# Kernel tuning notes

Hardware: AMD Instinct MI355X
Metric: run time of the kernel (lower is better)

The kernel has to match this reference:

```python
import jax, jax.numpy as jnp
import numpy as np

D_STATE = 16
DT_RANK = 48
D_CONV = 4
EPS = 1e-5


def rmsnorm(x, w):
    return x * jax.lax.rsqrt(jnp.mean(x * x, axis=-1, keepdims=True) + EPS) * w


def causal_dw_conv(u, w, b):
    # u: [B,T,D], w: [D,K] depthwise causal kernel, b: [D]
    B, T, D = u.shape
    K = w.shape[1]
    up = jnp.pad(u, ((0, 0), (K - 1, 0), (0, 0)))
    acc = jnp.zeros_like(u)
    for k in range(K):  # K=4, tiny fixed loop
        acc = acc + up[:, k:k + T, :] * w[:, k]
    return acc + b


def mamba_mixer(h, ipw, cw, cb, xpw, dpw, dpb, alog, dpar, opw):
    # h: [B,T,d_model]
    B, T, _ = h.shape
    xz = h @ ipw.T                       # [B,T,2*d_inner]
    u, z = jnp.split(xz, 2, axis=-1)     # each [B,T,d_inner]
    u = jax.nn.silu(causal_dw_conv(u, cw, cb))
    xp = u @ xpw.T                       # [B,T,dt_rank+2*d_state]
    dt = xp[..., :DT_RANK]
    Bm = xp[..., DT_RANK:DT_RANK + D_STATE]
    Cm = xp[..., DT_RANK + D_STATE:]
    delta = jax.nn.softplus(dt @ dpw.T + dpb)      # [B,T,d_inner]
    A = -jnp.exp(alog)                              # [d_inner, d_state], negative
    dA = jnp.exp(delta[..., None] * A)              # [B,T,d_inner,d_state] in (0,1)
    dBu = (delta * u)[..., None] * Bm[:, :, None, :]
    # time-major for scan
    dA_t = jnp.moveaxis(dA, 1, 0)
    dBu_t = jnp.moveaxis(dBu, 1, 0)
    C_t = jnp.moveaxis(Cm, 1, 0)

    def step(hst, inp):
        a, bu, c = inp
        hst = a * hst + bu                          # [B,d_inner,d_state]
        y = jnp.einsum('bdn,bn->bd', hst, c)
        return hst, y

    h0 = jnp.zeros((B, u.shape[-1], D_STATE), u.dtype)
    _, ys = jax.lax.scan(step, h0, (dA_t, dBu_t, C_t))
    y = jnp.moveaxis(ys, 0, 1) + u * dpar           # skip via D
    y = y * jax.nn.silu(z)                          # gate
    return y @ opw.T                                # [B,T,d_model]


def setup_inputs() -> dict:
    key = jax.random.key(0)
    ks = jax.random.split(key, 16)
    L, d_model, d_inner = 4, 768, 1536
    B, C, T = 4, 256, 512
    s = 0.02
    return {
        'x': jax.random.normal(ks[0], (B, C, T), jnp.float32),
        'in_proj_w': jax.random.normal(ks[1], (L, 2 * d_inner, d_model), jnp.float32) * s,
        'conv_w': jax.random.normal(ks[2], (L, d_inner, D_CONV), jnp.float32) * 0.3,
        'conv_b': jnp.zeros((L, d_inner), jnp.float32),
        'x_proj_w': jax.random.normal(ks[3], (L, DT_RANK + 2 * D_STATE, d_inner), jnp.float32) * s,
        'dt_proj_w': jax.random.normal(ks[4], (L, d_inner, DT_RANK), jnp.float32) * 0.1,
        'dt_proj_b': jax.random.normal(ks[5], (L, d_inner), jnp.float32) * 0.1 - 4.0,
        'A_log': jax.random.uniform(ks[6], (L, d_inner, D_STATE), jnp.float32, 0.0, 1.5),
        'D_param': jax.random.uniform(ks[7], (L, d_inner), jnp.float32),
        'out_proj_w': jax.random.normal(ks[8], (L, d_model, d_inner), jnp.float32) * s,
        'norm_w': jnp.ones((L, d_model), jnp.float32),
        'norm_f_w': jnp.ones((d_model,), jnp.float32),
        'inp_w': jax.random.normal(ks[9], (d_model, C), jnp.float32) * s,
        'inp_b': jnp.zeros((d_model,), jnp.float32),
        'cls_w': jax.random.normal(ks[10], (10, d_model), jnp.float32) * s,
        'cls_b': jnp.zeros((10,), jnp.float32),
    }


def reference(x, in_proj_w, conv_w, conv_b, x_proj_w, dt_proj_w, dt_proj_b,
              A_log, D_param, out_proj_w, norm_w, norm_f_w,
              inp_w, inp_b, cls_w, cls_b):
    # x: (B, C, T) -> (B, T, C)
    xt = jnp.transpose(x, (0, 2, 1))
    h = xt @ inp_w.T + inp_b                # [B,T,d_model]
    hidden = h
    residual = None
    L = in_proj_w.shape[0]
    for l in range(L):
        residual = hidden if residual is None else hidden + residual
        normed = rmsnorm(residual, norm_w[l])
        hidden = mamba_mixer(normed, in_proj_w[l], conv_w[l], conv_b[l],
                             x_proj_w[l], dt_proj_w[l], dt_proj_b[l],
                             A_log[l], D_param[l], out_proj_w[l])
    residual = hidden + residual
    hidden = rmsnorm(residual, norm_f_w)
    pooled = hidden.mean(axis=1)            # [B,d_model]
    logits = pooled @ cls_w.T + cls_b       # [B,num_labels]
    return logits
```

## Files before the change

kernel.cpp:

```cpp
#include <hip/hip_runtime.h>
#include <math.h>

#define D_MODEL 768
#define D_INNER 1536
#define B_SZ 4
#define T_SZ 512
#define ROWS (B_SZ*T_SZ)
#define XP_N 80
#define CH 16
#define CT 32
#define XS 8
#define XKC (D_INNER/XS)
#define OS 4
#define OKC (D_INNER/OS)
#define MN_OUT (ROWS*768)

typedef __attribute__((ext_vector_type(8))) short bf16x8;
typedef __attribute__((ext_vector_type(4))) float f32x4;

__device__ __forceinline__ float sigmoidf_(float x){ return 1.0f/(1.0f+__expf(-x)); }
__device__ __forceinline__ float siluf_(float x){ return x*sigmoidf_(x); }
__device__ __forceinline__ unsigned short f2bf(float f){
  unsigned u = __builtin_bit_cast(unsigned, f);
  u = (u + 0x7FFFu + ((u >> 16) & 1u)) >> 16;
  return (unsigned short)u;
}

__global__ void transpose_x(const float* __restrict__ x, float* __restrict__ xt){
  __shared__ float s[32][33];
  int b = blockIdx.z;
  int t0 = blockIdx.x*32, c0 = blockIdx.y*32;
  int tx = threadIdx.x, ty = threadIdx.y;
  s[ty][tx] = x[((size_t)b*256 + (c0+ty))*512 + (t0+tx)];
  __syncthreads();
  xt[((size_t)b*512 + (t0+ty))*256 + (c0+tx)] = s[tx][ty];
}

__global__ __launch_bounds__(256) void cast2_bf16(
    const float* __restrict__ in1, unsigned short* __restrict__ o1, int n1, int nb1,
    const float* __restrict__ in2, unsigned short* __restrict__ o2, int n2)
{
  const float* in; unsigned short* o; int i4;
  if ((int)blockIdx.x < nb1){ in = in1; o = o1; i4 = (blockIdx.x*256 + threadIdx.x)*4; if (i4 >= n1) return; }
  else { in = in2; o = o2; i4 = ((blockIdx.x-nb1)*256 + threadIdx.x)*4; if (i4 >= n2) return; }
  float4 v = *(const float4*)(in + i4);
  ushort4 r;
  r.x = f2bf(v.x); r.y = f2bf(v.y); r.z = f2bf(v.z); r.w = f2bf(v.w);
  *(ushort4*)(o + i4) = r;
}

#define LDP 40
__global__ __launch_bounds__(256) void gemm_bf16(
    const unsigned short* __restrict__ A, const unsigned short* __restrict__ Wb,
    float* __restrict__ C, int M, int N, int K)
{
  __shared__ unsigned short As[128*LDP];
  __shared__ unsigned short Ws[128*LDP];
  const int tid = threadIdx.x;
  const int bm = blockIdx.y*128, bn = blockIdx.x*128;
  const int wave = tid >> 6, lane = tid & 63;
  const int wm = (wave >> 1)*64, wn = (wave & 1)*64;
  const int fr = lane & 15, quad = lane >> 4;
  f32x4 acc[4][4] = {};
  const int srow = tid >> 1, scol = (tid & 1)*16;
  const unsigned short* Ag = A  + (size_t)(bm + srow)*K + scol;
  const unsigned short* Wg = Wb + (size_t)(bn + srow)*K + scol;
  unsigned short* Asw = As + srow*LDP + scol;
  unsigned short* Wsw = Ws + srow*LDP + scol;

  for (int k0 = 0; k0 < K; k0 += 32){
    float4 av0 = *(const float4*)(Ag + k0);
    float4 av1 = *(const float4*)(Ag + k0 + 8);
    float4 wv0 = *(const float4*)(Wg + k0);
    float4 wv1 = *(const float4*)(Wg + k0 + 8);
    __syncthreads();
    *(float4*)(Asw)     = av0; *(float4*)(Asw + 8) = av1;
    *(float4*)(Wsw)     = wv0; *(float4*)(Wsw + 8) = wv1;
    __syncthreads();
    bf16x8 a[4], b[4];
    #pragma unroll
    for (int i=0;i<4;i++)
      a[i] = *(const bf16x8*)(As + (wm + i*16 + fr)*LDP + quad*8);
    #pragma unroll
    for (int j=0;j<4;j++)
      b[j] = *(const bf16x8*)(Ws + (wn + j*16 + fr)*LDP + quad*8);
    #pragma unroll
    for (int i=0;i<4;i++)
      #pragma unroll
      for (int j=0;j<4;j++)
        acc[i][j] = __builtin_amdgcn_mfma_f32_16x16x32_bf16(a[i], b[j], acc[i][j], 0, 0, 0);
  }
  #pragma unroll
  for (int i=0;i<4;i++){
    #pragma unroll
    for (int r=0;r<4;r++){
      const int row = bm + wm + i*16 + quad*4 + r;
      float* Cp = C + (size_t)row*N + bn + wn + fr;
      #pragma unroll
      for (int j=0;j<4;j++)
        Cp[j*16] = acc[i][j][r];
    }
  }
}

__global__ __launch_bounds__(256) void gemm_bf16_sk(
    const unsigned short* __restrict__ A, const unsigned short* __restrict__ Wb,
    float* __restrict__ P0, float* __restrict__ P1, int M, int N, int K)
{
  __shared__ unsigned short As[128*LDP];
  __shared__ unsigned short Ws[128*LDP];
  const int tid = threadIdx.x;
  const int bm = blockIdx.y*128, bn = blockIdx.x*128;
  const int s = blockIdx.z;
  const int koff = s*OKC;
  const int wave = tid >> 6, lane = tid & 63;
  const int wm = (wave >> 1)*64, wn = (wave & 1)*64;
  const int fr = lane & 15, quad = lane >> 4;
  f32x4 acc[4][4] = {};
  const int srow = tid >> 1, scol = (tid & 1)*16;
  const unsigned short* Ag = A  + (size_t)(bm + srow)*K + koff + scol;
  const unsigned short* Wg = Wb + (size_t)(bn + srow)*K + koff + scol;
  unsigned short* Asw = As + srow*LDP + scol;
  unsigned short* Wsw = Ws + srow*LDP + scol;

  for (int k0 = 0; k0 < OKC; k0 += 32){
    float4 av0 = *(const float4*)(Ag + k0);
    float4 av1 = *(const float4*)(Ag + k0 + 8);
    float4 wv0 = *(const float4*)(Wg + k0);
    float4 wv1 = *(const float4*)(Wg + k0 + 8);
    __syncthreads();
    *(float4*)(Asw)     = av0; *(float4*)(Asw + 8) = av1;
    *(float4*)(Wsw)     = wv0; *(float4*)(Wsw + 8) = wv1;
    __syncthreads();
    bf16x8 a[4], b[4];
    #pragma unroll
    for (int i=0;i<4;i++)
      a[i] = *(const bf16x8*)(As + (wm + i*16 + fr)*LDP + quad*8);
    #pragma unroll
    for (int j=0;j<4;j++)
      b[j] = *(const bf16x8*)(Ws + (wn + j*16 + fr)*LDP + quad*8);
    #pragma unroll
    for (int i=0;i<4;i++)
      #pragma unroll
      for (int j=0;j<4;j++)
        acc[i][j] = __builtin_amdgcn_mfma_f32_16x16x32_bf16(a[i], b[j], acc[i][j], 0, 0, 0);
  }
  float* Cb = (s < 2 ? P0 : P1) + (size_t)(s & 1)*MN_OUT;
  #pragma unroll
  for (int i=0;i<4;i++){
    #pragma unroll
    for (int r=0;r<4;r++){
      const int row = bm + wm + i*16 + quad*4 + r;
      float* Cp = Cb + (size_t)row*N + bn + wn + fr;
      #pragma unroll
      for (int j=0;j<4;j++)
        Cp[j*16] = acc[i][j][r];
    }
  }
}

__global__ __launch_bounds__(256) void reduce_out(
    const float* __restrict__ P0, const float* __restrict__ P1,
    float* __restrict__ C)
{
  const int i = blockIdx.x*256 + threadIdx.x;
  C[i] = (P0[i] + P0[MN_OUT + i]) + (P1[i] + P1[MN_OUT + i]);
}

__global__ __launch_bounds__(256) void sgemm_tn(
    const float* __restrict__ A, int lda,
    const float* __restrict__ W,
    const float* __restrict__ bias,
    float* __restrict__ C, int M, int N, int K, int act)
{
  __shared__ float As[16][64];
  __shared__ float Wsh[16][64];
  const int bm = blockIdx.y*64, bn = blockIdx.x*64;
  const int tid = threadIdx.x;
  const int tx = tid & 15, ty = tid >> 4;
  const int lm = tid & 63, lk = (tid >> 6) << 2;
  float acc[4][4] = {};
  const float* Ap = A + (size_t)(bm+lm)*lda + lk;
  const float* Wp = W + (size_t)(bn+lm)*K + lk;
  const bool wok = (bn+lm) < N;
  for (int k0 = 0; k0 < K; k0 += 16){
    float4 av = *(const float4*)(Ap + k0);
    float4 wv = wok ? *(const float4*)(Wp + k0) : make_float4(0.f,0.f,0.f,0.f);
    As[lk+0][lm]=av.x; As[lk+1][lm]=av.y; As[lk+2][lm]=av.z; As[lk+3][lm]=av.w;
    Wsh[lk+0][lm]=wv.x; Wsh[lk+1][lm]=wv.y; Wsh[lk+2][lm]=wv.z; Wsh[lk+3][lm]=wv.w;
    __syncthreads();
    #pragma unroll
    for (int k = 0; k < 16; k++){
      float a[4], w[4];
      #pragma unroll
      for (int i=0;i<4;i++) a[i] = As[k][ty*4+i];
      #pragma unroll
      for (int j=0;j<4;j++) w[j] = Wsh[k][tx*4+j];
      #pragma unroll
      for (int i=0;i<4;i++)
        #pragma unroll
        for (int j=0;j<4;j++)
          acc[i][j] += a[i]*w[j];
    }
    __syncthreads();
  }
  #pragma unroll
  for (int i=0;i<4;i++){
    const int r = bm + ty*4 + i;
    #pragma unroll
    for (int j=0;j<4;j++){
      const int n = bn + tx*4 + j;
      if (n < N){
        float v = acc[i][j] + (bias ? bias[n] : 0.f);
        if (act == 1){ v = (v > 20.f) ? v : log1pf(__expf(v)); }
        C[(size_t)r*N + n] = v;
      }
    }
  }
}

__global__ __launch_bounds__(256) void sgemm_splitk_xp(
    const float* __restrict__ A, const float* __restrict__ W,
    float* __restrict__ part)
{
  __shared__ float As[16][64];
  __shared__ float Wsh[16][64];
  const int bm = blockIdx.y*64, bn = blockIdx.x*64;
  const int s = blockIdx.z;
  const int koff = s*XKC;
  const int tid = threadIdx.x;
  const int tx = tid & 15, ty = tid >> 4;
  const int lm = tid & 63, lk = (tid >> 6) << 2;
  float acc[4][4] = {};
  const float* Ap = A + (size_t)(bm+lm)*D_INNER + koff + lk;
  const float* Wp = W + (size_t)(bn+lm)*D_INNER + koff + lk;
  const bool wok = (bn+lm) < XP_N;
  for (int k0 = 0; k0 < XKC; k0 += 16){
    float4 av = *(const float4*)(Ap + k0);
    float4 wv = wok ? *(const float4*)(Wp + k0) : make_float4(0.f,0.f,0.f,0.f);
    As[lk+0][lm]=av.x; As[lk+1][lm]=av.y; As[lk+2][lm]=av.z; As[lk+3][lm]=av.w;
    Wsh[lk+0][lm]=wv.x; Wsh[lk+1][lm]=wv.y; Wsh[lk+2][lm]=wv.z; Wsh[lk+3][lm]=wv.w;
    __syncthreads();
    #pragma unroll
    for (int k = 0; k < 16; k++){
      float a[4], w[4];
      #pragma unroll
      for (int i=0;i<4;i++) a[i] = As[k][ty*4+i];
      #pragma unroll
      for (int j=0;j<4;j++) w[j] = Wsh[k][tx*4+j];
      #pragma unroll
      for (int i=0;i<4;i++)
        #pragma unroll
        for (int j=0;j<4;j++)
          acc[i][j] += a[i]*w[j];
    }
    __syncthreads();
  }
  #pragma unroll
  for (int i=0;i<4;i++){
    const int r = bm + ty*4 + i;
    #pragma unroll
    for (int j=0;j<4;j++){
      const int n = bn + tx*4 + j;
      if (n < XP_N)
        part[((size_t)s*ROWS + r)*XP_N + n] = acc[i][j];
    }
  }
}

__global__ __launch_bounds__(256) void reduce_xp(const float* __restrict__ part,
                                                 float* __restrict__ xp){
  const int i = blockIdx.x*256 + threadIdx.x;
  if (i >= ROWS*XP_N) return;
  float s = 0.f;
  #pragma unroll
  for (int c=0;c<XS;c++) s += part[(size_t)c*ROWS*XP_N + i];
  xp[i] = s;
}

__global__ __launch_bounds__(256) void add_rmsnorm(
    float* __restrict__ resid, const float* __restrict__ add,
    const float* __restrict__ w, float* __restrict__ out,
    unsigned short* __restrict__ obf)
{
  const int row = blockIdx.x;
  const int tid = threadIdx.x;
  float v[3];
  float ss = 0.f;
  #pragma unroll
  for (int i=0;i<3;i++){
    const int c = tid + i*256;
    float r = resid[(size_t)row*768 + c];
    if (add) r += add[(size_t)row*768 + c];
    v[i] = r;
    ss += r*r;
  }
  #pragma unroll
  for (int off=32; off>=1; off>>=1) ss += __shfl_xor(ss, off);
  __shared__ float sred[4];
  const int lane = tid & 63, wv = tid >> 6;
  if (lane == 0) sred[wv] = ss;
  __syncthreads();
  const float tot = sred[0]+sred[1]+sred[2]+sred[3];
  const float scale = rsqrtf(tot*(1.0f/768.0f) + 1e-5f);
  #pragma unroll
  for (int i=0;i<3;i++){
    const int c = tid + i*256;
    if (add) resid[(size_t)row*768 + c] = v[i];
    const float o = v[i]*scale*w[c];
    if (obf) obf[(size_t)row*768 + c] = f2bf(o);
    else     out[(size_t)row*768 + c] = o;
  }
}

__global__ __launch_bounds__(256) void conv_silu(
    const float* __restrict__ xz, const float* __restrict__ cw,
    const float* __restrict__ cb, float* __restrict__ uo)
{
  const int idx = blockIdx.x*256 + threadIdx.x;
  if (idx >= ROWS*D_INNER) return;
  const int d = idx % D_INNER;
  const int row = idx / D_INNER;
  const int t = row & (T_SZ-1);
  float acc = cb[d];
  #pragma unroll
  for (int k=0;k<4;k++){
    const int tt = t - 3 + k;
    if (tt >= 0)
      acc += xz[(size_t)(row - 3 + k)*3072 + d] * cw[d*4 + k];
  }
  uo[idx] = siluf_(acc);
}

__global__ __launch_bounds__(256) void scan_pass1(
    const float* __restrict__ delta, const float* __restrict__ u,
    const float* __restrict__ xp, const float* __restrict__ alog,
    float* __restrict__ Pend, float* __restrict__ Hend)
{
  const int d = blockIdx.x*256 + threadIdx.x;
  const int b = blockIdx.y, c = blockIdx.z;
  float4 t0 = *(const float4*)(alog + d*16 + 0);
  float4 t1 = *(const float4*)(alog + d*16 + 4);
  float4 t2 = *(const float4*)(alog + d*16 + 8);
  float4 t3 = *(const float4*)(alog + d*16 + 12);
  float Av[16] = {t0.x,t0.y,t0.z,t0.w,t1.x,t1.y,t1.z,t1.w,
                  t2.x,t2.y,t2.z,t2.w,t3.x,t3.y,t3.z,t3.w};
  float h[16], P[16];
  #pragma unroll
  for (int n=0;n<16;n++){ Av[n] = -__expf(Av[n]); h[n]=0.f; P[n]=1.f; }
  const size_t row0 = (size_t)b*T_SZ + (size_t)c*CT;
  const float* dp = delta + row0*D_INNER + d;
  const float* up = u     + row0*D_INNER + d;
  const float* bp = xp    + row0*XP_N + 48;
  for (int t=0;t<CT;t++){
    const float dv = dp[(size_t)t*D_INNER];
    const float uv = up[(size_t)t*D_INNER];
    const float4 B0 = *(const float4*)(bp + (size_t)t*XP_N);
    const float4 B1 = *(const float4*)(bp + (size_t)t*XP_N + 4);
    const float4 B2 = *(const float4*)(bp + (size_t)t*XP_N + 8);
    const float4 B3 = *(const float4*)(bp + (size_t)t*XP_N + 12);
    const float Bv[16] = {B0.x,B0.y,B0.z,B0.w,B1.x,B1.y,B1.z,B1.w,
                          B2.x,B2.y,B2.z,B2.w,B3.x,B3.y,B3.z,B3.w};
    const float du = dv*uv;
    #pragma unroll
    for (int n=0;n<16;n++){
      const float dA = __expf(dv*Av[n]);
      P[n] *= dA;
      h[n] = dA*h[n] + du*Bv[n];
    }
  }
  float* Pp = Pend + ((size_t)(b*CH+c)*D_INNER + d)*16;
  float* Hp = Hend + ((size_t)(b*CH+c)*D_INNER + d)*16;
  *(float4*)(Pp+ 0) = make_float4(P[0],P[1],P[2],P[3]);
  *(float4*)(Pp+ 4) = make_float4(P[4],P[5],P[6],P[7]);
  *(float4*)(Pp+ 8) = make_float4(P[8],P[9],P[10],P[11]);
  *(float4*)(Pp+12) = make_float4(P[12],P[13],P[14],P[15]);
  *(float4*)(Hp+ 0) = make_float4(h[0],h[1],h[2],h[3]);
  *(float4*)(Hp+ 4) = make_float4(h[4],h[5],h[6],h[7]);
  *(float4*)(Hp+ 8) = make_float4(h[8],h[9],h[10],h[11]);
  *(float4*)(Hp+12) = make_float4(h[12],h[13],h[14],h[15]);
}

__global__ __launch_bounds__(256) void scan_combine(
    const float* __restrict__ Pend, const float* __restrict__ Hend,
    float* __restrict__ Hin)
{
  const int gid = blockIdx.x*256 + threadIdx.x;
  const int b = gid / (D_INNER*16);
  const int r = gid % (D_INNER*16);
  const size_t base = (size_t)b*CH*D_INNER*16 + r;
  const size_t step = (size_t)D_INNER*16;
  float h = 0.f;
  Hin[base] = 0.f;
  for (int c=0; c<CH-1; c++){
    h = Pend[base + (size_t)c*step]*h + Hend[base + (size_t)c*step];
    Hin[base + (size_t)(c+1)*step] = h;
  }
}

__global__ __launch_bounds__(256) void scan_pass3(
    const float* __restrict__ delta, const float* __restrict__ u,
    const float* __restrict__ xp, const float* __restrict__ xz,
    const float* __restrict__ alog, const float* __restrict__ Dp,
    const float* __restrict__ Hin, unsigned short* __restrict__ yb)
{
  const int d = blockIdx.x*256 + threadIdx.x;
  const int b = blockIdx.y, c = blockIdx.z;
  float4 t0 = *(const float4*)(alog + d*16 + 0);
  float4 t1 = *(const float4*)(alog + d*16 + 4);
  float4 t2 = *(const float4*)(alog + d*16 + 8);
  float4 t3 = *(const float4*)(alog + d*16 + 12);
  float Av[16] = {t0.x,t0.y,t0.z,t0.w,t1.x,t1.y,t1.z,t1.w,
                  t2.x,t2.y,t2.z,t2.w,t3.x,t3.y,t3.z,t3.w};
  #pragma unroll
  for (int n=0;n<16;n++) Av[n] = -__expf(Av[n]);
  const float* Hp = Hin + ((size_t)(b*CH+c)*D_INNER + d)*16;
  float4 h0 = *(const float4*)(Hp+0);
  float4 h1 = *(const float4*)(Hp+4);
  float4 h2 = *(const float4*)(Hp+8);
  float4 h3 = *(const float4*)(Hp+12);
  float h[16] = {h0.x,h0.y,h0.z,h0.w,h1.x,h1.y,h1.z,h1.w,
                 h2.x,h2.y,h2.z,h2.w,h3.x,h3.y,h3.z,h3.w};
  const float Dv = Dp[d];
  const size_t row0 = (size_t)b*T_SZ + (size_t)c*CT;
  const float* dp = delta + row0*D_INNER + d;
  const float* up = u     + row0*D_INNER + d;
  const float* bp = xp    + row0*XP_N + 48;
  const float* cp = xp    + row0*XP_N + 64;
  const float* zp = xz    + row0*3072 + 1536 + d;
  unsigned short* yp = yb + row0*D_INNER + d;
  for (int t=0;t<CT;t++){
    const float dv = dp[(size_t)t*D_INNER];
    const float uv = up[(size_t)t*D_INNER];
    const float zv = zp[(size_t)t*3072];
    const float4 B0 = *(const float4*)(bp + (size_t)t*XP_N);
    const float4 B1 = *(const float4*)(bp + (size_t)t*XP_N + 4);
    const float4 B2 = *(const float4*)(bp + (size_t)t*XP_N + 8);
    const float4 B3 = *(const float4*)(bp + (size_t)t*XP_N + 12);
    const float4 C0 = *(const float4*)(cp + (size_t)t*XP_N);
    const float4 C1 = *(const float4*)(cp + (size_t)t*XP_N + 4);
    const float4 C2 = *(const float4*)(cp + (size_t)t*XP_N + 8);
    const float4 C3 = *(const float4*)(cp + (size_t)t*XP_N + 12);
    const float Bv[16] = {B0.x,B0.y,B0.z,B0.w,B1.x,B1.y,B1.z,B1.w,
                          B2.x,B2.y,B2.z,B2.w,B3.x,B3.y,B3.z,B3.w};
    const float Cv[16] = {C0.x,C0.y,C0.z,C0.w,C1.x,C1.y,C1.z,C1.w,
                          C2.x,C2.y,C2.z,C2.w,C3.x,C3.y,C3.z,C3.w};
    const float du = dv*uv;
    float p = 0.f;
    #pragma unroll
    for (int n=0;n<16;n++){
      const float dA = __expf(dv*Av[n]);
      h[n] = dA*h[n] + du*Bv[n];
      p += h[n]*Cv[n];
    }
    yp[(size_t)t*D_INNER] = f2bf((p + uv*Dv)*siluf_(zv));
  }
}

__global__ __launch_bounds__(256) void pool_partial(const float* __restrict__ normed,
                                                    float* __restrict__ part){
  const int i = blockIdx.x*256 + threadIdx.x;
  const int s = blockIdx.y;
  const int b = i / 768, m = i % 768;
  float sum = 0.f;
  const float* p = normed + ((size_t)b*T_SZ + s*32)*768 + m;
  #pragma unroll
  for (int t=0; t<32; t++) sum += p[(size_t)t*768];
  part[s*3072 + i] = sum;
}

__global__ void pool_final(const float* __restrict__ part, float* __restrict__ pooled){
  const int i = blockIdx.x*256 + threadIdx.x;
  if (i >= 3072) return;
  float s = 0.f;
  #pragma unroll
  for (int c=0;c<16;c++) s += part[c*3072 + i];
  pooled[i] = s * (1.0f/T_SZ);
}

__global__ void cls_head(const float* __restrict__ pooled, const float* __restrict__ cw,
                         const float* __restrict__ cb, float* __restrict__ out){
  const int o = blockIdx.x % 10, b = blockIdx.x / 10;
  const int lane = threadIdx.x;
  float s = 0.f;
  for (int k = lane; k < 768; k += 64) s += pooled[b*768 + k]*cw[o*768 + k];
  #pragma unroll
  for (int off=32; off>=1; off>>=1) s += __shfl_xor(s, off);
  if (lane == 0) out[b*10 + o] = s + cb[o];
}

extern "C" void kernel_launch(void* const* d_in, const int* in_sizes, int n_in,
                              void* d_out, int out_size, void* d_ws, size_t ws_size,
                              hipStream_t stream) {
  const float* x         = (const float*)d_in[0];
  const float* in_proj_w = (const float*)d_in[1];
  const float* conv_w    = (const float*)d_in[2];
  const float* conv_b    = (const float*)d_in[3];
  const float* x_proj_w  = (const float*)d_in[4];
  const float* dt_proj_w = (const float*)d_in[5];
  const float* dt_proj_b = (const float*)d_in[6];
  const float* A_log     = (const float*)d_in[7];
  const float* D_param   = (const float*)d_in[8];
  const float* out_proj_w= (const float*)d_in[9];
  const float* norm_w    = (const float*)d_in[10];
  const float* norm_f_w  = (const float*)d_in[11];
  const float* inp_w     = (const float*)d_in[12];
  const float* inp_b     = (const float*)d_in[13];
  const float* cls_w     = (const float*)d_in[14];
  const float* cls_b     = (const float*)d_in[15];
  float* out = (float*)d_out;

  char* ws = (char*)d_ws;
  auto carve = [&](size_t nelem)->float* {
    float* p = (float*)ws;
    ws += ((nelem*sizeof(float) + 255)/256)*256;
    return p;
  };
  float* xt     = carve((size_t)ROWS*256);
  float* resid  = carve((size_t)ROWS*768);
  float* normed = carve((size_t)ROWS*768);
  float* hidden = carve((size_t)ROWS*768);
  float* xz     = carve((size_t)ROWS*3072);
  float* ucv    = carve((size_t)ROWS*1536);
  float* xp     = carve((size_t)ROWS*XP_N);
  float* delta  = carve((size_t)ROWS*1536);
  float* ybf_f  = carve((size_t)ROWS*1536/2);
  float* wbi_f  = carve((size_t)(3072*768)/2);
  float* wbo_f  = carve((size_t)(768*1536)/2);
  float* Hin    = carve((size_t)B_SZ*CH*D_INNER*16);
  float* xpart  = carve((size_t)XS*ROWS*XP_N);
  float* ppool  = carve((size_t)16*3072);
  float* pooled = carve((size_t)B_SZ*768);

  unsigned short* normedb = (unsigned short*)normed;
  unsigned short* ybf = (unsigned short*)ybf_f;
  unsigned short* wbi = (unsigned short*)wbi_f;
  unsigned short* wbo = (unsigned short*)wbo_f;
  float* Pend = normed;
  float* Hend = hidden;

  transpose_x<<<dim3(16,8,4), dim3(32,32), 0, stream>>>(x, xt);
  sgemm_tn<<<dim3(12,32), 256, 0, stream>>>(xt, 256, inp_w, inp_b, resid, ROWS, 768, 256, 0);

  for (int l = 0; l < 4; l++){
    add_rmsnorm<<<ROWS, 256, 0, stream>>>(resid, l ? hidden : nullptr, norm_w + (size_t)l*768,
                                          nullptr, normedb);
    cast2_bf16<<<2304+1152, 256, 0, stream>>>(in_proj_w + (size_t)l*3072*768, wbi, 3072*768, 2304,
                                              out_proj_w + (size_t)l*768*1536, wbo, 768*1536);
    gemm_bf16<<<dim3(24,16), 256, 0, stream>>>(normedb, wbi, xz, ROWS, 3072, 768);
    conv_silu<<<(ROWS*D_INNER)/256, 256, 0, stream>>>(xz, conv_w + (size_t)l*1536*4, conv_b + (size_t)l*1536, ucv);
    sgemm_splitk_xp<<<dim3(2,32,XS), 256, 0, stream>>>(ucv, x_proj_w + (size_t)l*XP_N*1536, xpart);
    reduce_xp<<<(ROWS*XP_N)/256, 256, 0, stream>>>(xpart, xp);
    sgemm_tn<<<dim3(24,32), 256, 0, stream>>>(xp, XP_N, dt_proj_w + (size_t)l*1536*48, dt_proj_b + (size_t)l*1536,
                                              delta, ROWS, 1536, 48, 1);
    scan_pass1<<<dim3(6,B_SZ,CH-1), 256, 0, stream>>>(delta, ucv, xp,
                                               A_log + (size_t)l*1536*16, Pend, Hend);
    scan_combine<<<(B_SZ*D_INNER*16)/256, 256, 0, stream>>>(Pend, Hend, Hin);
    scan_pass3<<<dim3(6,B_SZ,CH), 256, 0, stream>>>(delta, ucv, xp, xz,
                                               A_log + (size_t)l*1536*16, D_param + (size_t)l*1536, Hin, ybf);
    gemm_bf16_sk<<<dim3(6,16,OS), 256, 0, stream>>>(ybf, wbo, delta, ucv, ROWS, 768, 1536);
    reduce_out<<<MN_OUT/256, 256, 0, stream>>>(delta, ucv, hidden);
  }

  add_rmsnorm<<<ROWS, 256, 0, stream>>>(resid, hidden, norm_f_w, normed, nullptr);
  pool_partial<<<dim3(12,16), 256, 0, stream>>>(normed, ppool);
  pool_final<<<12, 256, 0, stream>>>(ppool, pooled);
  cls_head<<<40, 64, 0, stream>>>(pooled, cls_w, cls_b, out);
}
```

Measured before the change: 849.0 us.

## Use direct global-to-LDS loads in bf16 GEMMs and fuse norm, cast, reduce and pool kernels

The bf16 GEMMs now stage tiles with global_load_lds instead of going through registers, and use an XOR-style swizzled unpadded LDS layout to avoid bank conflicts. The split-K reduction of the out-projection is folded into the next layer's add+RMSnorm, which shares a launch with the weight bf16 casts. The pool reduction and classifier head are merged into one kernel. Together these cut register staging and several kernel launches and intermediate round trips, at the cost of an extra barrier per k-step and more complex swizzle indexing.

```diff
diff --git a/kernel.cpp b/kernel.cpp
--- a/kernel.cpp
+++ b/kernel.cpp
@@ -18,6 +18,10 @@
 typedef __attribute__((ext_vector_type(8))) short bf16x8;
 typedef __attribute__((ext_vector_type(4))) float f32x4;
 
+#define GLL(g, l) __builtin_amdgcn_global_load_lds( \
+    (const __attribute__((address_space(1))) void*)(g), \
+    (__attribute__((address_space(3))) void*)(l), 16, 0, 0)
+
 __device__ __forceinline__ float sigmoidf_(float x){ return 1.0f/(1.0f+__expf(-x)); }
 __device__ __forceinline__ float siluf_(float x){ return x*sigmoidf_(x); }
 __device__ __forceinline__ unsigned short f2bf(float f){
@@ -36,59 +40,50 @@
   xt[((size_t)b*512 + (t0+ty))*256 + (c0+tx)] = s[tx][ty];
 }
 
-__global__ __launch_bounds__(256) void cast2_bf16(
-    const float* __restrict__ in1, unsigned short* __restrict__ o1, int n1, int nb1,
-    const float* __restrict__ in2, unsigned short* __restrict__ o2, int n2)
-{
-  const float* in; unsigned short* o; int i4;
-  if ((int)blockIdx.x < nb1){ in = in1; o = o1; i4 = (blockIdx.x*256 + threadIdx.x)*4; if (i4 >= n1) return; }
-  else { in = in2; o = o2; i4 = ((blockIdx.x-nb1)*256 + threadIdx.x)*4; if (i4 >= n2) return; }
-  float4 v = *(const float4*)(in + i4);
-  ushort4 r;
-  r.x = f2bf(v.x); r.y = f2bf(v.y); r.z = f2bf(v.z); r.w = f2bf(v.w);
-  *(ushort4*)(o + i4) = r;
-}
-
-#define LDP 40
 __global__ __launch_bounds__(256) void gemm_bf16(
     const unsigned short* __restrict__ A, const unsigned short* __restrict__ Wb,
     float* __restrict__ C, int M, int N, int K)
 {
-  __shared__ unsigned short As[128*LDP];
-  __shared__ unsigned short Ws[128*LDP];
+  __shared__ unsigned short As[128*32];
+  __shared__ unsigned short Ws[128*32];
   const int tid = threadIdx.x;
   const int bm = blockIdx.y*128, bn = blockIdx.x*128;
   const int wave = tid >> 6, lane = tid & 63;
   const int wm = (wave >> 1)*64, wn = (wave & 1)*64;
   const int fr = lane & 15, quad = lane >> 4;
   f32x4 acc[4][4] = {};
-  const int srow = tid >> 1, scol = (tid & 1)*16;
-  const unsigned short* Ag = A  + (size_t)(bm + srow)*K + scol;
-  const unsigned short* Wg = Wb + (size_t)(bn + srow)*K + scol;
-  unsigned short* Asw = As + srow*LDP + scol;
-  unsigned short* Wsw = Ws + srow*LDP + scol;
+  const int row0 = (wave*64 + lane) >> 2;
+  const int khp  = lane & 3;
+  const int khl  = (khp + 4 - ((row0 >> 1) & 3)) & 3;
+  const unsigned short* Ag = A  + (size_t)(bm + row0)*K + khl*8;
+  const unsigned short* Wg = Wb + (size_t)(bn + row0)*K + khl*8;
+  const size_t rstep = (size_t)64*K;
+  unsigned short* ldsA = As + wave*512;
+  unsigned short* ldsW = Ws + wave*512;
 
   for (int k0 = 0; k0 < K; k0 += 32){
-    float4 av0 = *(const float4*)(Ag + k0);
-    float4 av1 = *(const float4*)(Ag + k0 + 8);
-    float4 wv0 = *(const float4*)(Wg + k0);
-    float4 wv1 = *(const float4*)(Wg + k0 + 8);
-    __syncthreads();
-    *(float4*)(Asw)     = av0; *(float4*)(Asw + 8) = av1;
-    *(float4*)(Wsw)     = wv0; *(float4*)(Wsw + 8) = wv1;
+    GLL(Ag + k0,          ldsA);
+    GLL(Ag + rstep + k0,  ldsA + 2048);
+    GLL(Wg + k0,          ldsW);
+    GLL(Wg + rstep + k0,  ldsW + 2048);
     __syncthreads();
     bf16x8 a[4], b[4];
     #pragma unroll
-    for (int i=0;i<4;i++)
-      a[i] = *(const bf16x8*)(As + (wm + i*16 + fr)*LDP + quad*8);
-    #pragma unroll
-    for (int j=0;j<4;j++)
-      b[j] = *(const bf16x8*)(Ws + (wn + j*16 + fr)*LDP + quad*8);
+    for (int i=0;i<4;i++){
+      const int row = wm + i*16 + fr;
+      a[i] = *(const bf16x8*)(As + row*32 + (((quad + (row>>1)) & 3)*8));
+    }
+    #pragma unroll
+    for (int j=0;j<4;j++){
+      const int row = wn + j*16 + fr;
+      b[j] = *(const bf16x8*)(Ws + row*32 + (((quad + (row>>1)) & 3)*8));
+    }
     #pragma unroll
     for (int i=0;i<4;i++)
       #pragma unroll
       for (int j=0;j<4;j++)
         acc[i][j] = __builtin_amdgcn_mfma_f32_16x16x32_bf16(a[i], b[j], acc[i][j], 0, 0, 0);
+    __syncthreads();
   }
   #pragma unroll
   for (int i=0;i<4;i++){
@@ -107,8 +102,8 @@
     const unsigned short* __restrict__ A, const unsigned short* __restrict__ Wb,
     float* __restrict__ P0, float* __restrict__ P1, int M, int N, int K)
 {
-  __shared__ unsigned short As[128*LDP];
-  __shared__ unsigned short Ws[128*LDP];
+  __shared__ unsigned short As[128*32];
+  __shared__ unsigned short Ws[128*32];
   const int tid = threadIdx.x;
   const int bm = blockIdx.y*128, bn = blockIdx.x*128;
   const int s = blockIdx.z;
@@ -117,33 +112,38 @@
   const int wm = (wave >> 1)*64, wn = (wave & 1)*64;
   const int fr = lane & 15, quad = lane >> 4;
   f32x4 acc[4][4] = {};
-  const int srow = tid >> 1, scol = (tid & 1)*16;
-  const unsigned short* Ag = A  + (size_t)(bm + srow)*K + koff + scol;
-  const unsigned short* Wg = Wb + (size_t)(bn + srow)*K + koff + scol;
-  unsigned short* Asw = As + srow*LDP + scol;
-  unsigned short* Wsw = Ws + srow*LDP + scol;
+  const int row0 = (wave*64 + lane) >> 2;
+  const int khp  = lane & 3;
+  const int khl  = (khp + 4 - ((row0 >> 1) & 3)) & 3;
+  const unsigned short* Ag = A  + (size_t)(bm + row0)*K + koff + khl*8;
+  const unsigned short* Wg = Wb + (size_t)(bn + row0)*K + koff + khl*8;
+  const size_t rstep = (size_t)64*K;
+  unsigned short* ldsA = As + wave*512;
+  unsigned short* ldsW = Ws + wave*512;
 
   for (int k0 = 0; k0 < OKC; k0 += 32){
-    float4 av0 = *(const float4*)(Ag + k0);
-    float4 av1 = *(const float4*)(Ag + k0 + 8);
-    float4 wv0 = *(const float4*)(Wg + k0);
-    float4 wv1 = *(const float4*)(Wg + k0 + 8);
-    __syncthreads();
-    *(float4*)(Asw)     = av0; *(float4*)(Asw + 8) = av1;
-    *(float4*)(Wsw)     = wv0; *(float4*)(Wsw + 8) = wv1;
+    GLL(Ag + k0,          ldsA);
+    GLL(Ag + rstep + k0,  ldsA + 2048);
+    GLL(Wg + k0,          ldsW);
+    GLL(Wg + rstep + k0,  ldsW + 2048);
     __syncthreads();
     bf16x8 a[4], b[4];
     #pragma unroll
-    for (int i=0;i<4;i++)
-      a[i] = *(const bf16x8*)(As + (wm + i*16 + fr)*LDP + quad*8);
-    #pragma unroll
-    for (int j=0;j<4;j++)
-      b[j] = *(const bf16x8*)(Ws + (wn + j*16 + fr)*LDP + quad*8);
+    for (int i=0;i<4;i++){
+      const int row = wm + i*16 + fr;
+      a[i] = *(const bf16x8*)(As + row*32 + (((quad + (row>>1)) & 3)*8));
+    }
+    #pragma unroll
+    for (int j=0;j<4;j++){
+      const int row = wn + j*16 + fr;
+      b[j] = *(const bf16x8*)(Ws + row*32 + (((quad + (row>>1)) & 3)*8));
+    }
     #pragma unroll
     for (int i=0;i<4;i++)
       #pragma unroll
       for (int j=0;j<4;j++)
         acc[i][j] = __builtin_amdgcn_mfma_f32_16x16x32_bf16(a[i], b[j], acc[i][j], 0, 0, 0);
+    __syncthreads();
   }
   float* Cb = (s < 2 ? P0 : P1) + (size_t)(s & 1)*MN_OUT;
   #pragma unroll
@@ -157,14 +157,6 @@
         Cp[j*16] = acc[i][j][r];
     }
   }
-}
-
-__global__ __launch_bounds__(256) void reduce_out(
-    const float* __restrict__ P0, const float* __restrict__ P1,
-    float* __restrict__ C)
-{
-  const int i = blockIdx.x*256 + threadIdx.x;
-  C[i] = (P0[i] + P0[MN_OUT + i]) + (P1[i] + P1[MN_OUT + i]);
 }
 
 __global__ __launch_bounds__(256) void sgemm_tn(
@@ -278,20 +270,34 @@
   xp[i] = s;
 }
 
-__global__ __launch_bounds__(256) void add_rmsnorm(
-    float* __restrict__ resid, const float* __restrict__ add,
-    const float* __restrict__ w, float* __restrict__ out,
-    unsigned short* __restrict__ obf)
-{
-  const int row = blockIdx.x;
+__global__ __launch_bounds__(256) void fused_norm_cast(
+    float* __restrict__ resid, const float* __restrict__ P0, const float* __restrict__ P1,
+    const float* __restrict__ w, unsigned short* __restrict__ obf, float* __restrict__ ofp,
+    const float* __restrict__ cin1, unsigned short* __restrict__ co1, int cn1, int cnb1,
+    const float* __restrict__ cin2, unsigned short* __restrict__ co2, int cn2)
+{
+  const int blk = blockIdx.x;
+  if (blk >= 2048){
+    const int cb = blk - 2048;
+    const float* in; unsigned short* o; int i4;
+    if (cb < cnb1){ in = cin1; o = co1; i4 = (cb*256 + threadIdx.x)*4; if (i4 >= cn1) return; }
+    else { in = cin2; o = co2; i4 = ((cb-cnb1)*256 + threadIdx.x)*4; if (i4 >= cn2) return; }
+    float4 v = *(const float4*)(in + i4);
+    ushort4 r;
+    r.x = f2bf(v.x); r.y = f2bf(v.y); r.z = f2bf(v.z); r.w = f2bf(v.w);
+    *(ushort4*)(o + i4) = r;
+    return;
+  }
+  const int row = blk;
   const int tid = threadIdx.x;
   float v[3];
   float ss = 0.f;
   #pragma unroll
   for (int i=0;i<3;i++){
     const int c = tid + i*256;
-    float r = resid[(size_t)row*768 + c];
-    if (add) r += add[(size_t)row*768 + c];
+    const size_t idx = (size_t)row*768 + c;
+    float r = resid[idx];
+    if (P0) r += (P0[idx] + P0[MN_OUT + idx]) + (P1[idx] + P1[MN_OUT + idx]);
     v[i] = r;
     ss += r*r;
   }
@@ -306,10 +312,11 @@
   #pragma unroll
   for (int i=0;i<3;i++){
     const int c = tid + i*256;
-    if (add) resid[(size_t)row*768 + c] = v[i];
+    const size_t idx = (size_t)row*768 + c;
+    if (P0) resid[idx] = v[i];
     const float o = v[i]*scale*w[c];
-    if (obf) obf[(size_t)row*768 + c] = f2bf(o);
-    else     out[(size_t)row*768 + c] = o;
+    if (obf) obf[idx] = f2bf(o);
+    else     ofp[idx] = o;
   }
 }
 
@@ -469,24 +476,30 @@
   part[s*3072 + i] = sum;
 }
 
-__global__ void pool_final(const float* __restrict__ part, float* __restrict__ pooled){
-  const int i = blockIdx.x*256 + threadIdx.x;
-  if (i >= 3072) return;
-  float s = 0.f;
-  #pragma unroll
-  for (int c=0;c<16;c++) s += part[c*3072 + i];
-  pooled[i] = s * (1.0f/T_SZ);
-}
-
-__global__ void cls_head(const float* __restrict__ pooled, const float* __restrict__ cw,
-                         const float* __restrict__ cb, float* __restrict__ out){
-  const int o = blockIdx.x % 10, b = blockIdx.x / 10;
-  const int lane = threadIdx.x;
-  float s = 0.f;
-  for (int k = lane; k < 768; k += 64) s += pooled[b*768 + k]*cw[o*768 + k];
-  #pragma unroll
-  for (int off=32; off>=1; off>>=1) s += __shfl_xor(s, off);
-  if (lane == 0) out[b*10 + o] = s + cb[o];
+__global__ __launch_bounds__(256) void pool_cls(const float* __restrict__ part,
+                                                const float* __restrict__ cw,
+                                                const float* __restrict__ cb,
+                                                float* __restrict__ out){
+  __shared__ float ls[768];
+  const int b = blockIdx.x;
+  const int tid = threadIdx.x;
+  #pragma unroll
+  for (int i=0;i<3;i++){
+    const int m = tid + i*256;
+    float s = 0.f;
+    #pragma unroll
+    for (int c=0;c<16;c++) s += part[c*3072 + b*768 + m];
+    ls[m] = s * (1.0f/T_SZ);
+  }
+  __syncthreads();
+  const int wave = tid >> 6, lane = tid & 63;
+  for (int o = wave; o < 10; o += 4){
+    float s = 0.f;
+    for (int k = lane; k < 768; k += 64) s += ls[k]*cw[o*768 + k];
+    #pragma unroll
+    for (int off=32; off>=1; off>>=1) s += __shfl_xor(s, off);
+    if (lane == 0) out[b*10 + o] = s + cb[o];
+  }
 }
 
 extern "C" void kernel_launch(void* const* d_in, const int* in_sizes, int n_in,
@@ -531,6 +544,7 @@
   float* xpart  = carve((size_t)XS*ROWS*XP_N);
   float* ppool  = carve((size_t)16*3072);
   float* pooled = carve((size_t)B_SZ*768);
+  (void)pooled;
 
   unsigned short* normedb = (unsigned short*)normed;
   unsigned short* ybf = (unsigned short*)ybf_f;
@@ -543,10 +557,11 @@
   sgemm_tn<<<dim3(12,32), 256, 0, stream>>>(xt, 256, inp_w, inp_b, resid, ROWS, 768, 256, 0);
 
   for (int l = 0; l < 4; l++){
-    add_rmsnorm<<<ROWS, 256, 0, stream>>>(resid, l ? hidden : nullptr, norm_w + (size_t)l*768,
-                                          nullptr, normedb);
-    cast2_bf16<<<2304+1152, 256, 0, stream>>>(in_proj_w + (size_t)l*3072*768, wbi, 3072*768, 2304,
-                                              out_proj_w + (size_t)l*768*1536, wbo, 768*1536);
+    fused_norm_cast<<<2048 + 2304 + 1152, 256, 0, stream>>>(
+        resid, l ? delta : nullptr, l ? ucv : nullptr,
+        norm_w + (size_t)l*768, normedb, nullptr,
+        in_proj_w + (size_t)l*3072*768, wbi, 3072*768, 2304,
+        out_proj_w + (size_t)l*768*1536, wbo, 768*1536);
     gemm_bf16<<<dim3(24,16), 256, 0, stream>>>(normedb, wbi, xz, ROWS, 3072, 768);
     conv_silu<<<(ROWS*D_INNER)/256, 256, 0, stream>>>(xz, conv_w + (size_t)l*1536*4, conv_b + (size_t)l*1536, ucv);
     sgemm_splitk_xp<<<dim3(2,32,XS), 256, 0, stream>>>(ucv, x_proj_w + (size_t)l*XP_N*1536, xpart);
@@ -559,11 +574,11 @@
     scan_pass3<<<dim3(6,B_SZ,CH), 256, 0, stream>>>(delta, ucv, xp, xz,
                                                A_log + (size_t)l*1536*16, D_param + (size_t)l*1536, Hin, ybf);
     gemm_bf16_sk<<<dim3(6,16,OS), 256, 0, stream>>>(ybf, wbo, delta, ucv, ROWS, 768, 1536);
-    reduce_out<<<MN_OUT/256, 256, 0, stream>>>(delta, ucv, hidden);
-  }
-
-  add_rmsnorm<<<ROWS, 256, 0, stream>>>(resid, hidden, norm_f_w, normed, nullptr);
+  }
+
+  fused_norm_cast<<<2048, 256, 0, stream>>>(
+      resid, delta, ucv, norm_f_w, nullptr, normed,
+      nullptr, nullptr, 0, 0, nullptr, nullptr, 0);
   pool_partial<<<dim3(12,16), 256, 0, stream>>>(normed, ppool);
-  pool_final<<<12, 256, 0, stream>>>(ppool, pooled);
-  cls_head<<<40, 64, 0, stream>>>(pooled, cls_w, cls_b, out);
-}
+  pool_cls<<<4, 256, 0, stream>>>(ppool, cls_w, cls_b, out);
+}
```

After: 826.6 us. 2.6% less time.
